# Performance work log

Measured on AMD Instinct MI355X. Metric: run time of the kernel, lower is better.

## Reference

```python
import jax, jax.numpy as jnp
import numpy as np

BATCH = 16384
NUM_JOINTS = 21
TOKEN_DIM = 128
NUM_HEADS = 8
HEAD_DIM = TOKEN_DIM // NUM_HEADS
FF_DIM = TOKEN_DIM * 2
EPS = 1e-5

# MediaPipe 21-joint hand skeleton edges
SKELETON_EDGES = [(0,1),(1,2),(2,3),(3,4),(0,5),(5,6),(6,7),(7,8),(0,9),(9,10),
                  (10,11),(11,12),(0,13),(13,14),(14,15),(15,16),(0,17),(17,18),(18,19),(19,20)]

def build_adjacency_mask():
    m = np.eye(NUM_JOINTS, dtype=bool)
    for a, b in SKELETON_EDGES:
        m[a, b] = True
        m[b, a] = True
    return jnp.asarray(m)

def layer_norm(x, gamma, beta):
    mu = jnp.mean(x, axis=-1, keepdims=True)
    var = jnp.mean(jnp.square(x - mu), axis=-1, keepdims=True)
    return (x - mu) * jax.lax.rsqrt(var + EPS) * gamma + beta

def setup_inputs() -> dict:
    key = jax.random.key(0)
    ks = jax.random.split(key, 8)
    s = 0.02
    d = TOKEN_DIM
    return {
        "tokens": jax.random.normal(ks[0], (BATCH, NUM_JOINTS, d), jnp.float32),
        "Wq": jax.random.normal(ks[1], (d, d), jnp.float32) * s, "bq": jnp.zeros((d,), jnp.float32),
        "Wk": jax.random.normal(ks[2], (d, d), jnp.float32) * s, "bk": jnp.zeros((d,), jnp.float32),
        "Wv": jax.random.normal(ks[3], (d, d), jnp.float32) * s, "bv": jnp.zeros((d,), jnp.float32),
        "Wo": jax.random.normal(ks[4], (d, d), jnp.float32) * s, "bo": jnp.zeros((d,), jnp.float32),
        "g1": jnp.ones((d,), jnp.float32), "beta1": jnp.zeros((d,), jnp.float32),
        "g2": jnp.ones((d,), jnp.float32), "beta2": jnp.zeros((d,), jnp.float32),
        "W1": jax.random.normal(ks[5], (d, FF_DIM), jnp.float32) * s, "bf1": jnp.zeros((FF_DIM,), jnp.float32),
        "W2": jax.random.normal(ks[6], (FF_DIM, d), jnp.float32) * s, "bf2": jnp.zeros((d,), jnp.float32),
    }

def reference(tokens, Wq, bq, Wk, bk, Wv, bv, Wo, bo, g1, beta1, g2, beta2, W1, bf1, W2, bf2):
    B, J, D = tokens.shape
    mask = build_adjacency_mask()  # [J, J] bool, static
    q = (tokens @ Wq + bq).reshape(B, J, NUM_HEADS, HEAD_DIM)
    k = (tokens @ Wk + bk).reshape(B, J, NUM_HEADS, HEAD_DIM)
    v = (tokens @ Wv + bv).reshape(B, J, NUM_HEADS, HEAD_DIM)
    scores = jnp.einsum('bqhd,bkhd->bhqk', q, k) / jnp.sqrt(jnp.float32(HEAD_DIM))
    scores = jnp.where(mask[None, None, :, :], scores, -jnp.inf)
    attn = jax.nn.softmax(scores, axis=-1)
    attended = jnp.einsum('bhqk,bkhd->bqhd', attn, v).reshape(B, J, D)
    attended = attended @ Wo + bo
    x = layer_norm(tokens + attended, g1, beta1)
    ff = jax.nn.relu(x @ W1 + bf1) @ W2 + bf2
    return layer_norm(x + ff, g2, beta2)
```

## Files before the change

kernel.cpp:

```cpp
#include <hip/hip_runtime.h>
#include <stdint.h>

#define BATCHN 16384
#define NJ 21
#define DIM 128
#define NH 8
#define FFD 256
#define BB 3

typedef __attribute__((ext_vector_type(8))) short short8;
typedef __attribute__((ext_vector_type(4))) float f32x4;

__device__ __forceinline__ ushort f2bf(float f) {
  uint32_t u = __builtin_bit_cast(uint32_t, f);
  u += 0x7fffu + ((u >> 16) & 1u);
  return (ushort)(u >> 16);
}
__device__ __forceinline__ float bf2f(ushort h) {
  return __builtin_bit_cast(float, (uint32_t)h << 16);
}

__device__ const int d_nbr[21][6] = {
  {0,1,5,9,13,17},{0,1,2,0,0,0},{1,2,3,0,0,0},{2,3,4,0,0,0},{3,4,0,0,0,0},
  {0,5,6,0,0,0},{5,6,7,0,0,0},{6,7,8,0,0,0},{7,8,0,0,0,0},
  {0,9,10,0,0,0},{9,10,11,0,0,0},{10,11,12,0,0,0},{11,12,0,0,0,0},
  {0,13,14,0,0,0},{13,14,15,0,0,0},{14,15,16,0,0,0},{15,16,0,0,0,0},
  {0,17,18,0,0,0},{17,18,19,0,0,0},{18,19,20,0,0,0},{19,20,0,0,0,0}};
__device__ const int d_ncnt[21] = {6,3,3,3,2,3,3,3,2,3,3,3,2,3,3,3,2,3,3,3,2};

__global__ void pack_w(const float* __restrict__ Wq, const float* __restrict__ Wk,
                       const float* __restrict__ Wv, const float* __restrict__ Wo,
                       const float* __restrict__ W1, const float* __restrict__ W2,
                       ushort* __restrict__ out) {
  int t = blockIdx.x * 256 + threadIdx.x;
  const float* W;
  int base, K, N, e;
  if (t < 65536) {
    int m = t >> 14;
    W = (m == 0) ? Wq : (m == 1) ? Wk : (m == 2) ? Wv : Wo;
    base = m << 14; K = 128; N = 128; e = t & 16383;
  } else if (t < 98304) {
    W = W1; base = 65536; K = 128; N = 256; e = t - 65536;
  } else {
    W = W2; base = 98304; K = 256; N = 128; e = t - 98304;
  }
  int kbc = K / 32;
  int nt = e / (kbc * 512);
  int rem = e - nt * (kbc * 512);
  int kb = rem >> 9;
  int l = (rem & 511) >> 3;
  int j = rem & 7;
  int k = kb * 32 + ((l >> 4) << 3) + j;
  int n = nt * 16 + (l & 15);
  out[base + e] = f2bf(W[k * N + n]);
}

template <int KBLKS, int NT_PER_WAVE, bool RELU>
__device__ __forceinline__ void gemm_tile(ushort* sm, int aBase, int aRS,
                                          int dBase, int dRS,
                                          const ushort* __restrict__ wp,
                                          const float* __restrict__ bias,
                                          int lane, int w) {
  short8 afr[4][KBLKS];
#pragma unroll
  for (int mt = 0; mt < 4; ++mt) {
#pragma unroll
    for (int kb = 0; kb < KBLKS; ++kb) {
      int r = mt * 16 + (lane & 15);
      int c = kb * 32 + ((lane >> 4) << 3);
      afr[mt][kb] = *(const short8*)&sm[aBase + r * aRS + (c ^ ((r & 7) << 3))];
    }
  }
#pragma unroll
  for (int i = 0; i < NT_PER_WAVE; ++i) {
    int nt = w + 4 * i;
    short8 bfr[KBLKS];
#pragma unroll
    for (int kb = 0; kb < KBLKS; ++kb)
      bfr[kb] = *(const short8*)&wp[(nt * KBLKS + kb) * 512 + lane * 8];
    int col = nt * 16 + (lane & 15);
    float bv = bias[col];
#pragma unroll
    for (int mt = 0; mt < 4; ++mt) {
      f32x4 acc = {0.f, 0.f, 0.f, 0.f};
#pragma unroll
      for (int kb = 0; kb < KBLKS; ++kb)
        acc = __builtin_amdgcn_mfma_f32_16x16x32_bf16(afr[mt][kb], bfr[kb], acc, 0, 0, 0);
#pragma unroll
      for (int i2 = 0; i2 < 4; ++i2) {
        int r = mt * 16 + ((lane >> 4) << 2) + i2;
        float v = acc[i2] + bv;
        if (RELU) v = fmaxf(v, 0.f);
        sm[dBase + r * dRS + (col ^ ((r & 7) << 3))] = f2bf(v);
      }
    }
  }
}

__global__ __launch_bounds__(256, 2)
void gat_fused(const float* __restrict__ tok, const ushort* __restrict__ wpk,
               const float* __restrict__ bq, const float* __restrict__ bk,
               const float* __restrict__ bv, const float* __restrict__ bo,
               const float* __restrict__ g1, const float* __restrict__ be1,
               const float* __restrict__ g2, const float* __restrict__ be2,
               const float* __restrict__ bf1, const float* __restrict__ bf2,
               float* __restrict__ out) {
  __shared__ ushort sm[32768];
  const int tid = threadIdx.x;
  const int lane = tid & 63, w = tid >> 6;
  const int gb = blockIdx.x * BB;
  const int nb = min(BB, BATCHN - gb);
  const int nrows = nb * NJ;
  const int R0 = 0, R1 = 8192, R2 = 16384, R3 = 24576;

  {
    const float4* tp = (const float4*)(tok + (size_t)gb * NJ * DIM);
    for (int i = tid; i < nrows * 16; i += 256) {
      int r = i >> 4, c8 = (i & 15) << 3;
      float4 fa = tp[2 * i], fb = tp[2 * i + 1];
      uint4 u;
      u.x = f2bf(fa.x) | ((uint32_t)f2bf(fa.y) << 16);
      u.y = f2bf(fa.z) | ((uint32_t)f2bf(fa.w) << 16);
      u.z = f2bf(fb.x) | ((uint32_t)f2bf(fb.y) << 16);
      u.w = f2bf(fb.z) | ((uint32_t)f2bf(fb.w) << 16);
      *(uint4*)&sm[R0 + r * DIM + (c8 ^ ((r & 7) << 3))] = u;
    }
  }
  __syncthreads();

  gemm_tile<4, 2, false>(sm, R0, DIM, R1, DIM, wpk, bq, lane, w);
  gemm_tile<4, 2, false>(sm, R0, DIM, R2, DIM, wpk + 16384, bk, lane, w);
  gemm_tile<4, 2, false>(sm, R0, DIM, R3, DIM, wpk + 32768, bv, lane, w);
  __syncthreads();

  for (int it = tid; it < nb * NH * NJ; it += 256) {
    int b = it / (NH * NJ);
    int rem = it - b * (NH * NJ);
    int h = rem / NJ;
    int q = rem - h * NJ;
    int r = b * NJ + q;
    int hc = h << 4;
    float qf[16], av[16];
#pragma unroll
    for (int hf = 0; hf < 2; ++hf) {
      short8 qv = *(const short8*)&sm[R1 + r * DIM + ((hc + hf * 8) ^ ((r & 7) << 3))];
#pragma unroll
      for (int j = 0; j < 8; ++j) qf[hf * 8 + j] = bf2f((ushort)qv[j]);
    }
    int cnt = d_ncnt[q];
    float sc[6];
#pragma unroll
    for (int n = 0; n < 6; ++n) {
      int rk = b * NJ + d_nbr[q][n];
      float d = 0.f;
#pragma unroll
      for (int hf = 0; hf < 2; ++hf) {
        short8 kv = *(const short8*)&sm[R2 + rk * DIM + ((hc + hf * 8) ^ ((rk & 7) << 3))];
#pragma unroll
        for (int j = 0; j < 8; ++j) d += qf[hf * 8 + j] * bf2f((ushort)kv[j]);
      }
      sc[n] = (n < cnt) ? d * 0.25f : -__builtin_inff();
    }
    float mx = sc[0];
#pragma unroll
    for (int n = 1; n < 6; ++n) mx = fmaxf(mx, sc[n]);
    float ssum = 0.f;
#pragma unroll
    for (int n = 0; n < 6; ++n) { sc[n] = __expf(sc[n] - mx); ssum += sc[n]; }
    float inv = 1.f / ssum;
#pragma unroll
    for (int j = 0; j < 16; ++j) av[j] = 0.f;
#pragma unroll
    for (int n = 0; n < 6; ++n) {
      int rk = b * NJ + d_nbr[q][n];
      float wgt = sc[n];
#pragma unroll
      for (int hf = 0; hf < 2; ++hf) {
        short8 vv = *(const short8*)&sm[R3 + rk * DIM + ((hc + hf * 8) ^ ((rk & 7) << 3))];
#pragma unroll
        for (int j = 0; j < 8; ++j) av[hf * 8 + j] += wgt * bf2f((ushort)vv[j]);
      }
    }
#pragma unroll
    for (int hf = 0; hf < 2; ++hf) {
      uint4 u;
      u.x = f2bf(av[hf * 8 + 0] * inv) | ((uint32_t)f2bf(av[hf * 8 + 1] * inv) << 16);
      u.y = f2bf(av[hf * 8 + 2] * inv) | ((uint32_t)f2bf(av[hf * 8 + 3] * inv) << 16);
      u.z = f2bf(av[hf * 8 + 4] * inv) | ((uint32_t)f2bf(av[hf * 8 + 5] * inv) << 16);
      u.w = f2bf(av[hf * 8 + 6] * inv) | ((uint32_t)f2bf(av[hf * 8 + 7] * inv) << 16);
      *(uint4*)&sm[R0 + r * DIM + ((hc + hf * 8) ^ ((r & 7) << 3))] = u;
    }
  }
  __syncthreads();

  gemm_tile<4, 2, false>(sm, R0, DIM, R1, DIM, wpk + 49152, bo, lane, w);
  __syncthreads();

  {
    int r = tid >> 2, qd = tid & 3;
    if (r < nrows) {
      float x[32];
      const float* trow = tok + ((size_t)(gb * NJ + r)) * DIM + qd * 32;
#pragma unroll
      for (int i = 0; i < 4; ++i) {
        int c = qd * 32 + i * 8;
        short8 pv = *(const short8*)&sm[R1 + r * DIM + (c ^ ((r & 7) << 3))];
        float4 t0 = *(const float4*)(trow + i * 8);
        float4 t1 = *(const float4*)(trow + i * 8 + 4);
        x[i * 8 + 0] = bf2f((ushort)pv[0]) + t0.x;
        x[i * 8 + 1] = bf2f((ushort)pv[1]) + t0.y;
        x[i * 8 + 2] = bf2f((ushort)pv[2]) + t0.z;
        x[i * 8 + 3] = bf2f((ushort)pv[3]) + t0.w;
        x[i * 8 + 4] = bf2f((ushort)pv[4]) + t1.x;
        x[i * 8 + 5] = bf2f((ushort)pv[5]) + t1.y;
        x[i * 8 + 6] = bf2f((ushort)pv[6]) + t1.z;
        x[i * 8 + 7] = bf2f((ushort)pv[7]) + t1.w;
      }
      float s = 0.f, s2 = 0.f;
#pragma unroll
      for (int j = 0; j < 32; ++j) { s += x[j]; s2 += x[j] * x[j]; }
      s += __shfl_xor(s, 1); s += __shfl_xor(s, 2);
      s2 += __shfl_xor(s2, 1); s2 += __shfl_xor(s2, 2);
      float mu = s * 0.0078125f;
      float var = s2 * 0.0078125f - mu * mu;
      float rstd = rsqrtf(var + 1e-5f);
#pragma unroll
      for (int i = 0; i < 4; ++i) {
        int c = qd * 32 + i * 8;
        float4 ga = *(const float4*)(g1 + c), gc = *(const float4*)(g1 + c + 4);
        float4 ba = *(const float4*)(be1 + c), bc = *(const float4*)(be1 + c + 4);
        float y0 = (x[i * 8 + 0] - mu) * rstd * ga.x + ba.x;
        float y1 = (x[i * 8 + 1] - mu) * rstd * ga.y + ba.y;
        float y2 = (x[i * 8 + 2] - mu) * rstd * ga.z + ba.z;
        float y3 = (x[i * 8 + 3] - mu) * rstd * ga.w + ba.w;
        float y4 = (x[i * 8 + 4] - mu) * rstd * gc.x + bc.x;
        float y5 = (x[i * 8 + 5] - mu) * rstd * gc.y + bc.y;
        float y6 = (x[i * 8 + 6] - mu) * rstd * gc.z + bc.z;
        float y7 = (x[i * 8 + 7] - mu) * rstd * gc.w + bc.w;
        uint4 u;
        u.x = f2bf(y0) | ((uint32_t)f2bf(y1) << 16);
        u.y = f2bf(y2) | ((uint32_t)f2bf(y3) << 16);
        u.z = f2bf(y4) | ((uint32_t)f2bf(y5) << 16);
        u.w = f2bf(y6) | ((uint32_t)f2bf(y7) << 16);
        *(uint4*)&sm[R2 + r * DIM + (c ^ ((r & 7) << 3))] = u;
      }
    }
  }
  __syncthreads();

  gemm_tile<4, 4, true>(sm, R2, DIM, 0, FFD, wpk + 65536, bf1, lane, w);
  __syncthreads();

  gemm_tile<8, 2, false>(sm, 0, FFD, R3, DIM, wpk + 98304, bf2, lane, w);
  __syncthreads();

  {
    int r = tid >> 2, qd = tid & 3;
    if (r < nrows) {
      float x[32];
#pragma unroll
      for (int i = 0; i < 4; ++i) {
        int c = qd * 32 + i * 8;
        short8 pv = *(const short8*)&sm[R3 + r * DIM + (c ^ ((r & 7) << 3))];
        short8 xv = *(const short8*)&sm[R2 + r * DIM + (c ^ ((r & 7) << 3))];
#pragma unroll
        for (int j = 0; j < 8; ++j)
          x[i * 8 + j] = bf2f((ushort)pv[j]) + bf2f((ushort)xv[j]);
      }
      float s = 0.f, s2 = 0.f;
#pragma unroll
      for (int j = 0; j < 32; ++j) { s += x[j]; s2 += x[j] * x[j]; }
      s += __shfl_xor(s, 1); s += __shfl_xor(s, 2);
      s2 += __shfl_xor(s2, 1); s2 += __shfl_xor(s2, 2);
      float mu = s * 0.0078125f;
      float var = s2 * 0.0078125f - mu * mu;
      float rstd = rsqrtf(var + 1e-5f);
      float* orow = out + ((size_t)(gb * NJ + r)) * DIM + qd * 32;
#pragma unroll
      for (int i = 0; i < 4; ++i) {
        int c = qd * 32 + i * 8;
        float4 ga = *(const float4*)(g2 + c), gc = *(const float4*)(g2 + c + 4);
        float4 ba = *(const float4*)(be2 + c), bc = *(const float4*)(be2 + c + 4);
        float4 o0, o1;
        o0.x = (x[i * 8 + 0] - mu) * rstd * ga.x + ba.x;
        o0.y = (x[i * 8 + 1] - mu) * rstd * ga.y + ba.y;
        o0.z = (x[i * 8 + 2] - mu) * rstd * ga.z + ba.z;
        o0.w = (x[i * 8 + 3] - mu) * rstd * ga.w + ba.w;
        o1.x = (x[i * 8 + 4] - mu) * rstd * gc.x + bc.x;
        o1.y = (x[i * 8 + 5] - mu) * rstd * gc.y + bc.y;
        o1.z = (x[i * 8 + 6] - mu) * rstd * gc.z + bc.z;
        o1.w = (x[i * 8 + 7] - mu) * rstd * gc.w + bc.w;
        *(float4*)(orow + i * 8) = o0;
        *(float4*)(orow + i * 8 + 4) = o1;
      }
    }
  }
}

extern "C" void kernel_launch(void* const* d_in, const int* in_sizes, int n_in,
                              void* d_out, int out_size, void* d_ws, size_t ws_size,
                              hipStream_t stream) {
  const float* tok = (const float*)d_in[0];
  const float* Wq = (const float*)d_in[1];
  const float* bq = (const float*)d_in[2];
  const float* Wk = (const float*)d_in[3];
  const float* bk = (const float*)d_in[4];
  const float* Wv = (const float*)d_in[5];
  const float* bv = (const float*)d_in[6];
  const float* Wo = (const float*)d_in[7];
  const float* bo = (const float*)d_in[8];
  const float* g1 = (const float*)d_in[9];
  const float* be1 = (const float*)d_in[10];
  const float* g2 = (const float*)d_in[11];
  const float* be2 = (const float*)d_in[12];
  const float* W1 = (const float*)d_in[13];
  const float* bf1 = (const float*)d_in[14];
  const float* W2 = (const float*)d_in[15];
  const float* bf2 = (const float*)d_in[16];
  ushort* wpk = (ushort*)d_ws;

  pack_w<<<dim3(512), dim3(256), 0, stream>>>(Wq, Wk, Wv, Wo, W1, W2, wpk);
  int nblk = (BATCHN + BB - 1) / BB;
  gat_fused<<<dim3(nblk), dim3(256), 0, stream>>>(
      tok, wpk, bq, bk, bv, bo, g1, be1, g2, be2, bf1, bf2, (float*)d_out);
}
```

Baseline: 545.4 us.

## Shrink LDS to three regions and raise occupancy to three blocks per CU

Cuts shared memory from 64KB to 48KB by keeping the Q projection and the second FFN GEMM outputs in registers until the input region can be overwritten. The three QKV projections now share a single load of the A fragments. Launch bounds move from 2 to 3 blocks per CU for more latency hiding. In exchange it adds barriers and register pressure, which the compiler may answer with spills under the tighter register budget.

```diff
diff --git a/kernel.cpp b/kernel.cpp
--- a/kernel.cpp
+++ b/kernel.cpp
@@ -97,7 +97,62 @@
   }
 }
 
-__global__ __launch_bounds__(256, 2)
+template <int KBLKS, int NT_PER_WAVE>
+__device__ __forceinline__ void gemm_regout(const ushort* sm, int aBase, int aRS,
+                                            const ushort* __restrict__ wp,
+                                            const float* __restrict__ bias,
+                                            int lane, int w,
+                                            f32x4 acc[NT_PER_WAVE][4]) {
+  short8 afr[4][KBLKS];
+#pragma unroll
+  for (int mt = 0; mt < 4; ++mt) {
+#pragma unroll
+    for (int kb = 0; kb < KBLKS; ++kb) {
+      int r = mt * 16 + (lane & 15);
+      int c = kb * 32 + ((lane >> 4) << 3);
+      afr[mt][kb] = *(const short8*)&sm[aBase + r * aRS + (c ^ ((r & 7) << 3))];
+    }
+  }
+#pragma unroll
+  for (int i = 0; i < NT_PER_WAVE; ++i) {
+    int nt = w + 4 * i;
+    short8 bfr[KBLKS];
+#pragma unroll
+    for (int kb = 0; kb < KBLKS; ++kb)
+      bfr[kb] = *(const short8*)&wp[(nt * KBLKS + kb) * 512 + lane * 8];
+    float bv = bias[nt * 16 + (lane & 15)];
+#pragma unroll
+    for (int mt = 0; mt < 4; ++mt) {
+      f32x4 a = {0.f, 0.f, 0.f, 0.f};
+#pragma unroll
+      for (int kb = 0; kb < KBLKS; ++kb)
+        a = __builtin_amdgcn_mfma_f32_16x16x32_bf16(afr[mt][kb], bfr[kb], a, 0, 0, 0);
+#pragma unroll
+      for (int i2 = 0; i2 < 4; ++i2) a[i2] += bv;
+      acc[i][mt] = a;
+    }
+  }
+}
+
+template <int NT_PER_WAVE>
+__device__ __forceinline__ void write_frags(ushort* sm, int dBase, int dRS,
+                                            int lane, int w,
+                                            const f32x4 acc[NT_PER_WAVE][4]) {
+#pragma unroll
+  for (int i = 0; i < NT_PER_WAVE; ++i) {
+    int col = (w + 4 * i) * 16 + (lane & 15);
+#pragma unroll
+    for (int mt = 0; mt < 4; ++mt) {
+#pragma unroll
+      for (int i2 = 0; i2 < 4; ++i2) {
+        int r = mt * 16 + ((lane >> 4) << 2) + i2;
+        sm[dBase + r * dRS + (col ^ ((r & 7) << 3))] = f2bf(acc[i][mt][i2]);
+      }
+    }
+  }
+}
+
+__global__ __launch_bounds__(256, 3)
 void gat_fused(const float* __restrict__ tok, const ushort* __restrict__ wpk,
                const float* __restrict__ bq, const float* __restrict__ bk,
                const float* __restrict__ bv, const float* __restrict__ bo,
@@ -105,13 +160,13 @@
                const float* __restrict__ g2, const float* __restrict__ be2,
                const float* __restrict__ bf1, const float* __restrict__ bf2,
                float* __restrict__ out) {
-  __shared__ ushort sm[32768];
+  __shared__ ushort sm[24576];
   const int tid = threadIdx.x;
   const int lane = tid & 63, w = tid >> 6;
   const int gb = blockIdx.x * BB;
   const int nb = min(BB, BATCHN - gb);
   const int nrows = nb * NJ;
-  const int R0 = 0, R1 = 8192, R2 = 16384, R3 = 24576;
+  const int R0 = 0, R1 = 8192, R2 = 16384;
 
   {
     const float4* tp = (const float4*)(tok + (size_t)gb * NJ * DIM);
@@ -128,9 +183,68 @@
   }
   __syncthreads();
 
-  gemm_tile<4, 2, false>(sm, R0, DIM, R1, DIM, wpk, bq, lane, w);
-  gemm_tile<4, 2, false>(sm, R0, DIM, R2, DIM, wpk + 16384, bk, lane, w);
-  gemm_tile<4, 2, false>(sm, R0, DIM, R3, DIM, wpk + 32768, bv, lane, w);
+  f32x4 qacc[2][4];
+  {
+    short8 afr[4][4];
+#pragma unroll
+    for (int mt = 0; mt < 4; ++mt) {
+#pragma unroll
+      for (int kb = 0; kb < 4; ++kb) {
+        int r = mt * 16 + (lane & 15);
+        int c = kb * 32 + ((lane >> 4) << 3);
+        afr[mt][kb] = *(const short8*)&sm[R0 + r * DIM + (c ^ ((r & 7) << 3))];
+      }
+    }
+#pragma unroll
+    for (int m = 0; m < 2; ++m) {
+      const ushort* wp = wpk + (m == 0 ? 16384 : 32768);
+      const float* bias = (m == 0) ? bk : bv;
+      int dBase = (m == 0) ? R1 : R2;
+#pragma unroll
+      for (int i = 0; i < 2; ++i) {
+        int nt = w + 4 * i;
+        short8 bfr[4];
+#pragma unroll
+        for (int kb = 0; kb < 4; ++kb)
+          bfr[kb] = *(const short8*)&wp[(nt * 4 + kb) * 512 + lane * 8];
+        int col = nt * 16 + (lane & 15);
+        float bvv = bias[col];
+#pragma unroll
+        for (int mt = 0; mt < 4; ++mt) {
+          f32x4 a = {0.f, 0.f, 0.f, 0.f};
+#pragma unroll
+          for (int kb = 0; kb < 4; ++kb)
+            a = __builtin_amdgcn_mfma_f32_16x16x32_bf16(afr[mt][kb], bfr[kb], a, 0, 0, 0);
+#pragma unroll
+          for (int i2 = 0; i2 < 4; ++i2) {
+            int r = mt * 16 + ((lane >> 4) << 2) + i2;
+            sm[dBase + r * DIM + (col ^ ((r & 7) << 3))] = f2bf(a[i2] + bvv);
+          }
+        }
+      }
+    }
+#pragma unroll
+    for (int i = 0; i < 2; ++i) {
+      int nt = w + 4 * i;
+      short8 bfr[4];
+#pragma unroll
+      for (int kb = 0; kb < 4; ++kb)
+        bfr[kb] = *(const short8*)&wpk[(nt * 4 + kb) * 512 + lane * 8];
+      float bvv = bq[nt * 16 + (lane & 15)];
+#pragma unroll
+      for (int mt = 0; mt < 4; ++mt) {
+        f32x4 a = {0.f, 0.f, 0.f, 0.f};
+#pragma unroll
+        for (int kb = 0; kb < 4; ++kb)
+          a = __builtin_amdgcn_mfma_f32_16x16x32_bf16(afr[mt][kb], bfr[kb], a, 0, 0, 0);
+#pragma unroll
+        for (int i2 = 0; i2 < 4; ++i2) a[i2] += bvv;
+        qacc[i][mt] = a;
+      }
+    }
+  }
+  __syncthreads();
+  write_frags<2>(sm, R0, DIM, lane, w, qacc);
   __syncthreads();
 
   for (int it = tid; it < nb * NH * NJ; it += 256) {
@@ -143,7 +257,7 @@
     float qf[16], av[16];
 #pragma unroll
     for (int hf = 0; hf < 2; ++hf) {
-      short8 qv = *(const short8*)&sm[R1 + r * DIM + ((hc + hf * 8) ^ ((r & 7) << 3))];
+      short8 qv = *(const short8*)&sm[R0 + r * DIM + ((hc + hf * 8) ^ ((r & 7) << 3))];
 #pragma unroll
       for (int j = 0; j < 8; ++j) qf[hf * 8 + j] = bf2f((ushort)qv[j]);
     }
@@ -155,7 +269,7 @@
       float d = 0.f;
 #pragma unroll
       for (int hf = 0; hf < 2; ++hf) {
-        short8 kv = *(const short8*)&sm[R2 + rk * DIM + ((hc + hf * 8) ^ ((rk & 7) << 3))];
+        short8 kv = *(const short8*)&sm[R1 + rk * DIM + ((hc + hf * 8) ^ ((rk & 7) << 3))];
 #pragma unroll
         for (int j = 0; j < 8; ++j) d += qf[hf * 8 + j] * bf2f((ushort)kv[j]);
       }
@@ -176,7 +290,7 @@
       float wgt = sc[n];
 #pragma unroll
       for (int hf = 0; hf < 2; ++hf) {
-        short8 vv = *(const short8*)&sm[R3 + rk * DIM + ((hc + hf * 8) ^ ((rk & 7) << 3))];
+        short8 vv = *(const short8*)&sm[R2 + rk * DIM + ((hc + hf * 8) ^ ((rk & 7) << 3))];
 #pragma unroll
         for (int j = 0; j < 8; ++j) av[hf * 8 + j] += wgt * bf2f((ushort)vv[j]);
       }
@@ -251,7 +365,10 @@
   gemm_tile<4, 4, true>(sm, R2, DIM, 0, FFD, wpk + 65536, bf1, lane, w);
   __syncthreads();
 
-  gemm_tile<8, 2, false>(sm, 0, FFD, R3, DIM, wpk + 98304, bf2, lane, w);
+  f32x4 p2acc[2][4];
+  gemm_regout<8, 2>(sm, 0, FFD, wpk + 98304, bf2, lane, w, p2acc);
+  __syncthreads();
+  write_frags<2>(sm, R0, DIM, lane, w, p2acc);
   __syncthreads();
 
   {
@@ -261,7 +378,7 @@
 #pragma unroll
       for (int i = 0; i < 4; ++i) {
         int c = qd * 32 + i * 8;
-        short8 pv = *(const short8*)&sm[R3 + r * DIM + (c ^ ((r & 7) << 3))];
+        short8 pv = *(const short8*)&sm[R0 + r * DIM + (c ^ ((r & 7) << 3))];
         short8 xv = *(const short8*)&sm[R2 + r * DIM + (c ^ ((r & 7) << 3))];
 #pragma unroll
         for (int j = 0; j < 8; ++j)
```

Result: slower. 631.2 us (+15.7%).
